# Kernel tuning notes

Measured on AMD Instinct MI355X. Metric: run time of the kernel, lower is better.

Reference implementation:

```python
import jax, jax.numpy as jnp
import numpy as np
import math

EMBED = 512
NUM_CLASSES = 100000
BATCH = 512
SCALE = 64.0
MARGIN = 0.5
COS_M = math.cos(MARGIN)
SIN_M = math.sin(MARGIN)
THRESHOLD = math.cos(math.pi - MARGIN)
MARGIN_MULT = math.sin(math.pi - MARGIN) * MARGIN
EPS = 1e-12  # F.normalize eps


def setup_inputs() -> dict:
    key = jax.random.key(0)
    k1, k2, k3 = jax.random.split(key, 3)
    embeddings = jax.random.normal(k1, (BATCH, EMBED), dtype=jnp.float32)
    labels = jax.random.randint(k2, (BATCH,), 0, NUM_CLASSES, dtype=jnp.int64)
    # xavier-uniform-like init for weight (num_classes, embedding_size)
    limit = math.sqrt(6.0 / (NUM_CLASSES + EMBED))
    weight = jax.random.uniform(k3, (NUM_CLASSES, EMBED), dtype=jnp.float32,
                                minval=-limit, maxval=limit)
    return {"embeddings": embeddings, "labels": labels, "weight": weight}


def _l2_normalize(x, axis):
    norm = jnp.sqrt(jnp.sum(x * x, axis=axis, keepdims=True))
    return x / jnp.maximum(norm, EPS)


def reference(embeddings, labels, weight):
    e = _l2_normalize(embeddings, axis=1)          # (B, D)
    w = _l2_normalize(weight, axis=1)              # (C, D)
    cosine = jnp.einsum('bd,cd->bc', e, w)         # (B, C)
    sine = jnp.sqrt(jnp.clip(1.0 - cosine * cosine, 0.0, None))
    phi = cosine * COS_M - sine * SIN_M
    # easy_margin=False branch
    phi = jnp.where(cosine > THRESHOLD, phi, cosine - MARGIN_MULT)
    one_hot = jax.nn.one_hot(labels, NUM_CLASSES, dtype=cosine.dtype)
    logits = SCALE * (one_hot * phi + (1.0 - one_hot) * cosine)
    logp = jax.nn.log_softmax(logits, axis=1)      # (B, C)
    nll = -jnp.take_along_axis(logp, labels[:, None], axis=1)[:, 0]
    return jnp.mean(nll)
```

## Files before the change

kernel.cpp:

```cpp
#include <hip/hip_runtime.h>
#include <hip/hip_bf16.h>
#include <math.h>

#define BATCH 512
#define EMBED 512
#define NCLS  100000
#define NT128 782
#define NCG   128
#define NBLK  256

typedef __attribute__((ext_vector_type(4)))  float f32x4;
typedef __attribute__((ext_vector_type(16))) float f32x16;
typedef __attribute__((ext_vector_type(2)))  long  i64x2;

constexpr float kCOS_M = 0.8775825618903728f;
constexpr float kSIN_M = 0.4794255386042030f;
constexpr float kTHR   = -0.8775825618903728f;
constexpr float kMM    = 0.2397127693021015f;

#define BARRIER() asm volatile("s_waitcnt lgkmcnt(0)\n\ts_barrier" ::: "memory")

__device__ __forceinline__ unsigned cvt4(float a, float b, float c, float d) {
  int v = __builtin_amdgcn_cvt_pk_fp8_f32(a, b, 0, false);
  v = __builtin_amdgcn_cvt_pk_fp8_f32(c, d, v, true);
  return (unsigned)v;
}

__global__ void knorm_e(const float* __restrict__ E, unsigned char* __restrict__ En8) {
  int r = blockIdx.x;
  int l = threadIdx.x;
  const f32x4* src = (const f32x4*)(E + r * EMBED);
  f32x4 a = src[2 * l], b = src[2 * l + 1];
  float ss = a.x*a.x + a.y*a.y + a.z*a.z + a.w*a.w
           + b.x*b.x + b.y*b.y + b.z*b.z + b.w*b.w;
#pragma unroll
  for (int d = 1; d < 64; d <<= 1) ss += __shfl_xor(ss, d);
  float s = 16.0f / fmaxf(sqrtf(ss), 1e-12f);
  uint2 pk;
  pk.x = cvt4(a.x * s, a.y * s, a.z * s, a.w * s);
  pk.y = cvt4(b.x * s, b.y * s, b.z * s, b.w * s);
  int slotL = (l & 1) * 16 + (l >> 2);
  int half  = (l >> 1) & 1;
  *(uint2*)(En8 + r * 512 + (((slotL ^ (r & 31)) << 4) | (half << 3))) = pk;
}

__global__ void klabel(const float* __restrict__ E, const float* __restrict__ W,
                       const int* __restrict__ labels,
                       float* __restrict__ lcos, float* __restrict__ lphi)
{
  int r = blockIdx.x * 8 + (threadIdx.x >> 6);
  int l = threadIdx.x & 63;
  int lbl = labels[r];
  const float* ep = E + (size_t)r * EMBED + l * 8;
  const float* wp = W + (size_t)lbl * EMBED + l * 8;
  f32x4 e0 = *(const f32x4*)ep, e1 = *(const f32x4*)(ep + 4);
  f32x4 w0 = *(const f32x4*)wp, w1 = *(const f32x4*)(wp + 4);
  float dot = e0.x*w0.x + e0.y*w0.y + e0.z*w0.z + e0.w*w0.w
            + e1.x*w1.x + e1.y*w1.y + e1.z*w1.z + e1.w*w1.w;
  float se = e0.x*e0.x + e0.y*e0.y + e0.z*e0.z + e0.w*e0.w
           + e1.x*e1.x + e1.y*e1.y + e1.z*e1.z + e1.w*e1.w;
  float sw = w0.x*w0.x + w0.y*w0.y + w0.z*w0.z + w0.w*w0.w
           + w1.x*w1.x + w1.y*w1.y + w1.z*w1.z + w1.w*w1.w;
#pragma unroll
  for (int d = 1; d < 64; d <<= 1) {
    dot += __shfl_xor(dot, d); se += __shfl_xor(se, d); sw += __shfl_xor(sw, d);
  }
  float cosv = dot / (fmaxf(sqrtf(se), 1e-12f) * fmaxf(sqrtf(sw), 1e-12f));
  float cc = fminf(fmaxf(cosv, -1.f), 1.f);
  float sine = sqrtf(fmaxf(1.f - cc * cc, 0.f));
  float phi = (cosv > kTHR) ? (cosv * kCOS_M - sine * kSIN_M) : (cosv - kMM);
  if (l == 0) { lcos[r] = 64.f * cosv; lphi[r] = 64.f * phi; }
}

__global__ __launch_bounds__(1024, 4) void kmain(
    const unsigned char* __restrict__ En8, const float* __restrict__ W,
    float* __restrict__ psum)
{
  __shared__ __align__(16) unsigned char Asm[256 * 512];
  __shared__ __align__(16) unsigned char Bsm[2][8192];
  __shared__ float rowsum[128];
  __shared__ float smemS[2][256];

  int bid = blockIdx.x;
  int xcd = bid & 7;
  int panel = (bid >> 3) & 1;
  int grp = bid >> 4;
  int cg = xcd | (grp << 3);

  int tid = threadIdx.x;
  int w = tid >> 6, l = tid & 63;
  int wr = w >> 1, wc = w & 1;
  int cl = l & 31, hi = l >> 5;
  int bcls = tid >> 3, bs3 = tid & 7;

  int nt = (NT128 - cg + 127) >> 7;
  int nph = nt * 8;

#pragma unroll
  for (int i = 0; i < 8; ++i) {
    int base = i * 16384 + w * 1024;
    __builtin_amdgcn_global_load_lds(
        (const __attribute__((address_space(1))) void*)(En8 + panel * 131072 + base + l * 16),
        (__attribute__((address_space(3))) void*)(&Asm[base]), 16, 0, 0);
  }

  float ssq = 0.f;
  const int boff = (bcls >> 6) * 4096
                 + ((bs3 & 1) * 2 + (bs3 >> 2)) * 1024
                 + (bcls & 63) * 16 + ((bs3 >> 1) & 1) * 8;

  f32x4 Ra0, Ra1, Rb0, Rb1;
  auto loadB = [&](int q, f32x4& v0, f32x4& v1) {
    int cls = (cg + ((q >> 3) << 7)) * 128 + bcls;
    if (cls >= NCLS) cls = NCLS - 1;
    const float* p = W + (size_t)cls * EMBED + (q & 7) * 64 + bs3 * 8;
    v0 = *(const f32x4*)p;
    v1 = *(const f32x4*)(p + 4);
  };
  auto writeB = [&](int buf, f32x4 v0, f32x4 v1) {
    float x0 = v0.x*128.f, x1 = v0.y*128.f, x2 = v0.z*128.f, x3 = v0.w*128.f;
    float x4 = v1.x*128.f, x5 = v1.y*128.f, x6 = v1.z*128.f, x7 = v1.w*128.f;
    ssq += x0*x0 + x1*x1 + x2*x2 + x3*x3 + x4*x4 + x5*x5 + x6*x6 + x7*x7;
    uint2 pk;
    pk.x = cvt4(x0, x1, x2, x3);
    pk.y = cvt4(x4, x5, x6, x7);
    *(uint2*)(&Bsm[buf][boff]) = pk;
  };

  f32x16 acc0, acc1, S;
#pragma unroll
  for (int e = 0; e < 16; ++e) { acc0[e] = 0.f; acc1[e] = 0.f; S[e] = 0.f; }

  const unsigned char* Abase = &Asm[(wr * 32 + cl) * 512];
  const unsigned char* Bc0 = &Bsm[0][wc * 4096 + (hi * 2) * 1024 + cl * 16];
  const unsigned char* Bc1 = &Bsm[1][wc * 4096 + (hi * 2) * 1024 + cl * 16];

  auto compute = [&](const unsigned char* bb, int pt) {
    int t0 = pt * 2;
    i64x2 a0 = *(const i64x2*)(Abase + ((((hi << 4) | t0)       ^ cl) << 4));
    i64x2 a1 = *(const i64x2*)(Abase + ((((hi << 4) | (t0 + 1)) ^ cl) << 4));
    i64x2 b0 = *(const i64x2*)(bb);
    i64x2 b1 = *(const i64x2*)(bb + 1024);
    i64x2 c0 = *(const i64x2*)(bb + 512);
    i64x2 c1 = *(const i64x2*)(bb + 1024 + 512);
    acc0 = __builtin_amdgcn_mfma_f32_32x32x16_fp8_fp8(a0[0], b0[0], acc0, 0, 0, 0);
    acc0 = __builtin_amdgcn_mfma_f32_32x32x16_fp8_fp8(a0[1], b0[1], acc0, 0, 0, 0);
    acc0 = __builtin_amdgcn_mfma_f32_32x32x16_fp8_fp8(a1[0], b1[0], acc0, 0, 0, 0);
    acc0 = __builtin_amdgcn_mfma_f32_32x32x16_fp8_fp8(a1[1], b1[1], acc0, 0, 0, 0);
    acc1 = __builtin_amdgcn_mfma_f32_32x32x16_fp8_fp8(a0[0], c0[0], acc1, 0, 0, 0);
    acc1 = __builtin_amdgcn_mfma_f32_32x32x16_fp8_fp8(a0[1], c0[1], acc1, 0, 0, 0);
    acc1 = __builtin_amdgcn_mfma_f32_32x32x16_fp8_fp8(a1[0], c1[0], acc1, 0, 0, 0);
    acc1 = __builtin_amdgcn_mfma_f32_32x32x16_fp8_fp8(a1[1], c1[1], acc1, 0, 0, 0);
  };

  auto ssqred = [&]() {
    float sq = ssq;
    sq += __shfl_xor(sq, 1); sq += __shfl_xor(sq, 2); sq += __shfl_xor(sq, 4);
    if (bs3 == 0) rowsum[bcls] = sq;
    ssq = 0.f;
  };

  auto epilogue = [&](int T) {
    int base = (cg + (T << 7)) * 128 + wc * 64;
    float rs0 = fmaxf(rowsum[wc * 64 + cl], 1e-30f);
    float rs1 = fmaxf(rowsum[wc * 64 + 32 + cl], 1e-30f);
    float rn0 = 4.0f / sqrtf(rs0);
    float rn1 = 4.0f / sqrtf(rs1);
    float vm0 = (base + cl < NCLS) ? 1.0f : 0.0f;
    float vm1 = (base + 32 + cl < NCLS) ? 1.0f : 0.0f;
#pragma unroll
    for (int e = 0; e < 16; ++e) {
      float u0 = __expf(fmaf(acc0[e], rn0, -64.0f));
      float u1 = __expf(fmaf(acc1[e], rn1, -64.0f));
      S[e] = fmaf(u0, vm0, fmaf(u1, vm1, S[e]));
      acc0[e] = 0.f; acc1[e] = 0.f;
    }
  };

  loadB(0, Ra0, Ra1); loadB(1, Rb0, Rb1);
  writeB(0, Ra0, Ra1); writeB(1, Rb0, Rb1);
  loadB(2, Ra0, Ra1); loadB(3, Rb0, Rb1);
  asm volatile("s_waitcnt vmcnt(0)" ::: "memory");
  BARRIER();

  for (int p = 0; p < nph; p += 2) {
    compute(Bc0, p & 7);
    BARRIER();
    if (p + 2 < nph) writeB(0, Ra0, Ra1);
    if (p + 4 < nph) loadB(p + 4, Ra0, Ra1);
    int po = p + 1;
    compute(Bc1, po & 7);
    if ((po & 7) == 7) epilogue(po >> 3);
    BARRIER();
    if (po + 2 < nph) writeB(1, Rb0, Rb1);
    if (po + 4 < nph) loadB(po + 4, Rb0, Rb1);
    if (((po + 2) & 7) == 7) ssqred();
  }

#pragma unroll
  for (int e = 0; e < 16; ++e) {
    float v = S[e];
    v += __shfl_xor(v, 1); v += __shfl_xor(v, 2); v += __shfl_xor(v, 4);
    v += __shfl_xor(v, 8); v += __shfl_xor(v, 16);
    S[e] = v;
  }
  __syncthreads();
  if (cl == 0) {
#pragma unroll
    for (int e = 0; e < 16; ++e) {
      int row = wr * 32 + (e & 3) + 8 * (e >> 2) + 4 * hi;
      smemS[wc][row] = S[e];
    }
  }
  __syncthreads();
  if (tid < 256) psum[bid * 256 + tid] = smemS[0][tid] + smemS[1][tid];
}

__global__ void kred1(const float* __restrict__ psum, float* __restrict__ pp2) {
  int g = blockIdx.x;
  int r = threadIdx.x;
  int panel = g >> 4, grp = g & 15;
  float s = 0.f;
#pragma unroll
  for (int x = 0; x < 8; ++x) {
    int bid = x | (panel << 3) | (grp << 4);
    s += psum[bid * 256 + r];
  }
  pp2[g * 256 + r] = s;
}

__global__ void kfinal(const float* __restrict__ pp2, const float* __restrict__ lcos,
                       const float* __restrict__ lphi, float* __restrict__ out)
{
  int tid = threadIdx.x;
  int panel = tid >> 8, rl = tid & 255;
  float S = 0.f;
#pragma unroll
  for (int grp = 0; grp < 16; ++grp)
    S += pp2[((panel << 4) | grp) * 256 + rl];
  float lc = lcos[tid], lp = lphi[tid];
  S = S - __expf(lc - 64.f) + __expf(lp - 64.f);
  float nll = 64.f + __logf(S) - lp;
#pragma unroll
  for (int d = 1; d < 64; d <<= 1) nll += __shfl_xor(nll, d);
  __shared__ float sm[8];
  if ((tid & 63) == 0) sm[tid >> 6] = nll;
  __syncthreads();
  if (tid == 0) {
    float t = 0.f;
    for (int k = 0; k < 8; ++k) t += sm[k];
    out[0] = t * (1.0f / 512.0f);
  }
}

extern "C" void kernel_launch(void* const* d_in, const int* in_sizes, int n_in,
                              void* d_out, int out_size, void* d_ws, size_t ws_size,
                              hipStream_t stream)
{
  const float* E      = (const float*)d_in[0];
  const int*   labels = (const int*)d_in[1];
  const float* W      = (const float*)d_in[2];
  float* out = (float*)d_out;

  char* ws = (char*)d_ws;
  unsigned char* En8 = (unsigned char*)ws;
  float* psum = (float*)(ws + 262144);
  float* pp2  = (float*)(ws + 524288);
  float* lcos = (float*)(ws + 557056);
  float* lphi = lcos + BATCH;

  knorm_e<<<BATCH, 64, 0, stream>>>(E, En8);
  klabel <<<64, 512, 0, stream>>>(E, W, labels, lcos, lphi);
  kmain  <<<NBLK, 1024, 0, stream>>>(En8, W, psum);
  kred1  <<<32, 256, 0, stream>>>(psum, pp2);
  kfinal <<<1, 512, 0, stream>>>(pp2, lcos, lphi, out);
}
```

Measured before the change: 80.83 us.

## Split batch into four 128-row panels and stream A tiles per phase

```diff
diff --git a/kernel.cpp b/kernel.cpp
--- a/kernel.cpp
+++ b/kernel.cpp
@@ -6,8 +6,7 @@
 #define EMBED 512
 #define NCLS  100000
 #define NT128 782
-#define NCG   128
-#define NBLK  256
+#define NBLK  512
 
 typedef __attribute__((ext_vector_type(4)))  float f32x4;
 typedef __attribute__((ext_vector_type(16))) float f32x16;
@@ -39,9 +38,8 @@
   uint2 pk;
   pk.x = cvt4(a.x * s, a.y * s, a.z * s, a.w * s);
   pk.y = cvt4(b.x * s, b.y * s, b.z * s, b.w * s);
-  int slotL = (l & 1) * 16 + (l >> 2);
-  int half  = (l >> 1) & 1;
-  *(uint2*)(En8 + r * 512 + (((slotL ^ (r & 31)) << 4) | (half << 3))) = pk;
+  int t = l >> 2, hi = l & 1, hf = (l >> 1) & 1;
+  *(uint2*)(En8 + ((((t << 1) | hi) * 512 + r) << 4) + hf * 8) = pk;
 }
 
 __global__ void klabel(const float* __restrict__ E, const float* __restrict__ W,
@@ -72,91 +70,99 @@
   if (l == 0) { lcos[r] = 64.f * cosv; lphi[r] = 64.f * phi; }
 }
 
-__global__ __launch_bounds__(1024, 4) void kmain(
+__global__ __launch_bounds__(512, 4) void kmain(
     const unsigned char* __restrict__ En8, const float* __restrict__ W,
     float* __restrict__ psum)
 {
-  __shared__ __align__(16) unsigned char Asm[256 * 512];
+  __shared__ __align__(16) unsigned char Asm[2][8192];
   __shared__ __align__(16) unsigned char Bsm[2][8192];
   __shared__ float rowsum[128];
-  __shared__ float smemS[2][256];
+  __shared__ float smemS[2][128];
 
   int bid = blockIdx.x;
   int xcd = bid & 7;
-  int panel = (bid >> 3) & 1;
-  int grp = bid >> 4;
+  int panel = (bid >> 3) & 3;
+  int grp = bid >> 5;
   int cg = xcd | (grp << 3);
 
   int tid = threadIdx.x;
   int w = tid >> 6, l = tid & 63;
   int wr = w >> 1, wc = w & 1;
   int cl = l & 31, hi = l >> 5;
-  int bcls = tid >> 3, bs3 = tid & 7;
-
-  int nt = (NT128 - cg + 127) >> 7;
+  int bcls = tid >> 2, bs = tid & 3;
+
+  int nt = (cg < 14) ? 7 : 6;
   int nph = nt * 8;
 
-#pragma unroll
-  for (int i = 0; i < 8; ++i) {
-    int base = i * 16384 + w * 1024;
+  int ac = tid >> 7, ar = tid & 127;
+  auto stageA = [&](int q) {
+    int t = ((q & 7) << 1) | (ac >> 1);
+    int hh = ac & 1;
+    const unsigned char* src = En8 + ((((t << 1) | hh) * 512 + panel * 128 + ar) << 4);
     __builtin_amdgcn_global_load_lds(
-        (const __attribute__((address_space(1))) void*)(En8 + panel * 131072 + base + l * 16),
-        (__attribute__((address_space(3))) void*)(&Asm[base]), 16, 0, 0);
-  }
+        (const __attribute__((address_space(1))) void*)src,
+        (__attribute__((address_space(3))) void*)(&Asm[q & 1][tid * 16]), 16, 0, 0);
+  };
 
   float ssq = 0.f;
-  const int boff = (bcls >> 6) * 4096
-                 + ((bs3 & 1) * 2 + (bs3 >> 2)) * 1024
-                 + (bcls & 63) * 16 + ((bs3 >> 1) & 1) * 8;
-
-  f32x4 Ra0, Ra1, Rb0, Rb1;
-  auto loadB = [&](int q, f32x4& v0, f32x4& v1) {
-    int cls = (cg + ((q >> 3) << 7)) * 128 + bcls;
+  const int tp = bs >> 1, hf = bs & 1;
+  const int wbase0 = (((tp << 1) | 0) * 128 + bcls) * 16 + hf * 8;
+  const int wbase1 = wbase0 + 2048;
+
+  f32x4 Ra[4], Rb[4];
+  auto loadB = [&](int q, f32x4* R) {
+    int T = q >> 3;
+    int cls = (cg + (T << 7)) * 128 + bcls;
     if (cls >= NCLS) cls = NCLS - 1;
-    const float* p = W + (size_t)cls * EMBED + (q & 7) * 64 + bs3 * 8;
-    v0 = *(const f32x4*)p;
-    v1 = *(const f32x4*)(p + 4);
-  };
-  auto writeB = [&](int buf, f32x4 v0, f32x4 v1) {
-    float x0 = v0.x*128.f, x1 = v0.y*128.f, x2 = v0.z*128.f, x3 = v0.w*128.f;
-    float x4 = v1.x*128.f, x5 = v1.y*128.f, x6 = v1.z*128.f, x7 = v1.w*128.f;
-    ssq += x0*x0 + x1*x1 + x2*x2 + x3*x3 + x4*x4 + x5*x5 + x6*x6 + x7*x7;
-    uint2 pk;
-    pk.x = cvt4(x0, x1, x2, x3);
-    pk.y = cvt4(x4, x5, x6, x7);
-    *(uint2*)(&Bsm[buf][boff]) = pk;
+    const float* p = W + (size_t)cls * EMBED + ((q & 7) << 6) + (bs << 4);
+#pragma unroll
+    for (int i = 0; i < 4; ++i) R[i] = *(const f32x4*)(p + i * 4);
+  };
+  auto writeB = [&](int buf, f32x4* R) {
+#pragma unroll
+    for (int i = 0; i < 4; ++i)
+      ssq += R[i].x*R[i].x + R[i].y*R[i].y + R[i].z*R[i].z + R[i].w*R[i].w;
+    uint2 p0, p1;
+    p0.x = cvt4(R[0].x*128.f, R[0].y*128.f, R[0].z*128.f, R[0].w*128.f);
+    p0.y = cvt4(R[1].x*128.f, R[1].y*128.f, R[1].z*128.f, R[1].w*128.f);
+    p1.x = cvt4(R[2].x*128.f, R[2].y*128.f, R[2].z*128.f, R[2].w*128.f);
+    p1.y = cvt4(R[3].x*128.f, R[3].y*128.f, R[3].z*128.f, R[3].w*128.f);
+    *(uint2*)(&Bsm[buf][wbase0]) = p0;
+    *(uint2*)(&Bsm[buf][wbase1]) = p1;
   };
 
   f32x16 acc0, acc1, S;
 #pragma unroll
   for (int e = 0; e < 16; ++e) { acc0[e] = 0.f; acc1[e] = 0.f; S[e] = 0.f; }
 
-  const unsigned char* Abase = &Asm[(wr * 32 + cl) * 512];
-  const unsigned char* Bc0 = &Bsm[0][wc * 4096 + (hi * 2) * 1024 + cl * 16];
-  const unsigned char* Bc1 = &Bsm[1][wc * 4096 + (hi * 2) * 1024 + cl * 16];
-
-  auto compute = [&](const unsigned char* bb, int pt) {
-    int t0 = pt * 2;
-    i64x2 a0 = *(const i64x2*)(Abase + ((((hi << 4) | t0)       ^ cl) << 4));
-    i64x2 a1 = *(const i64x2*)(Abase + ((((hi << 4) | (t0 + 1)) ^ cl) << 4));
-    i64x2 b0 = *(const i64x2*)(bb);
-    i64x2 b1 = *(const i64x2*)(bb + 1024);
-    i64x2 c0 = *(const i64x2*)(bb + 512);
-    i64x2 c1 = *(const i64x2*)(bb + 1024 + 512);
-    acc0 = __builtin_amdgcn_mfma_f32_32x32x16_fp8_fp8(a0[0], b0[0], acc0, 0, 0, 0);
-    acc0 = __builtin_amdgcn_mfma_f32_32x32x16_fp8_fp8(a0[1], b0[1], acc0, 0, 0, 0);
-    acc0 = __builtin_amdgcn_mfma_f32_32x32x16_fp8_fp8(a1[0], b1[0], acc0, 0, 0, 0);
-    acc0 = __builtin_amdgcn_mfma_f32_32x32x16_fp8_fp8(a1[1], b1[1], acc0, 0, 0, 0);
-    acc1 = __builtin_amdgcn_mfma_f32_32x32x16_fp8_fp8(a0[0], c0[0], acc1, 0, 0, 0);
-    acc1 = __builtin_amdgcn_mfma_f32_32x32x16_fp8_fp8(a0[1], c0[1], acc1, 0, 0, 0);
-    acc1 = __builtin_amdgcn_mfma_f32_32x32x16_fp8_fp8(a1[0], c1[0], acc1, 0, 0, 0);
-    acc1 = __builtin_amdgcn_mfma_f32_32x32x16_fp8_fp8(a1[1], c1[1], acc1, 0, 0, 0);
+  const int aoff = hi * 2048 + (wr * 32 + cl) * 16;
+  const int boff = hi * 2048 + (wc * 64 + cl) * 16;
+
+  auto compute = [&](int buf) {
+    const unsigned char* A = &Asm[buf][0];
+    const unsigned char* B = &Bsm[buf][0];
+    i64x2 a0  = *(const i64x2*)(A + aoff);
+    i64x2 a1  = *(const i64x2*)(A + aoff + 4096);
+    i64x2 b00 = *(const i64x2*)(B + boff);
+    i64x2 b01 = *(const i64x2*)(B + boff + 512);
+    i64x2 b10 = *(const i64x2*)(B + boff + 4096);
+    i64x2 b11 = *(const i64x2*)(B + boff + 4096 + 512);
+    __builtin_amdgcn_s_setprio(1);
+    acc0 = __builtin_amdgcn_mfma_f32_32x32x16_fp8_fp8(a0[0], b00[0], acc0, 0, 0, 0);
+    acc0 = __builtin_amdgcn_mfma_f32_32x32x16_fp8_fp8(a0[1], b00[1], acc0, 0, 0, 0);
+    acc1 = __builtin_amdgcn_mfma_f32_32x32x16_fp8_fp8(a0[0], b01[0], acc1, 0, 0, 0);
+    acc1 = __builtin_amdgcn_mfma_f32_32x32x16_fp8_fp8(a0[1], b01[1], acc1, 0, 0, 0);
+    acc0 = __builtin_amdgcn_mfma_f32_32x32x16_fp8_fp8(a1[0], b10[0], acc0, 0, 0, 0);
+    acc0 = __builtin_amdgcn_mfma_f32_32x32x16_fp8_fp8(a1[1], b10[1], acc0, 0, 0, 0);
+    acc1 = __builtin_amdgcn_mfma_f32_32x32x16_fp8_fp8(a1[0], b11[0], acc1, 0, 0, 0);
+    acc1 = __builtin_amdgcn_mfma_f32_32x32x16_fp8_fp8(a1[1], b11[1], acc1, 0, 0, 0);
+    __builtin_amdgcn_s_setprio(0);
   };
 
   auto ssqred = [&]() {
     float sq = ssq;
-    sq += __shfl_xor(sq, 1); sq += __shfl_xor(sq, 2); sq += __shfl_xor(sq, 4);
-    if (bs3 == 0) rowsum[bcls] = sq;
+    sq += __shfl_xor(sq, 1); sq += __shfl_xor(sq, 2);
+    if (bs == 0) rowsum[bcls] = sq;
     ssq = 0.f;
   };
 
@@ -164,8 +170,8 @@
     int base = (cg + (T << 7)) * 128 + wc * 64;
     float rs0 = fmaxf(rowsum[wc * 64 + cl], 1e-30f);
     float rs1 = fmaxf(rowsum[wc * 64 + 32 + cl], 1e-30f);
-    float rn0 = 4.0f / sqrtf(rs0);
-    float rn1 = 4.0f / sqrtf(rs1);
+    float rn0 = 0.03125f * rsqrtf(rs0);
+    float rn1 = 0.03125f * rsqrtf(rs1);
     float vm0 = (base + cl < NCLS) ? 1.0f : 0.0f;
     float vm1 = (base + 32 + cl < NCLS) ? 1.0f : 0.0f;
 #pragma unroll
@@ -177,24 +183,28 @@
     }
   };
 
-  loadB(0, Ra0, Ra1); loadB(1, Rb0, Rb1);
-  writeB(0, Ra0, Ra1); writeB(1, Rb0, Rb1);
-  loadB(2, Ra0, Ra1); loadB(3, Rb0, Rb1);
+  stageA(0);
+  loadB(0, Ra); loadB(1, Rb);
   asm volatile("s_waitcnt vmcnt(0)" ::: "memory");
+  writeB(0, Ra);
+  loadB(2, Ra);
   BARRIER();
 
   for (int p = 0; p < nph; p += 2) {
-    compute(Bc0, p & 7);
+    writeB(1, Rb);
+    stageA(p + 1);
+    loadB(p + 3, Rb);
+    if (((p + 1) & 7) == 7) ssqred();
+    asm volatile("s_waitcnt vmcnt(4)" ::: "memory");
+    compute(0);
     BARRIER();
-    if (p + 2 < nph) writeB(0, Ra0, Ra1);
-    if (p + 4 < nph) loadB(p + 4, Ra0, Ra1);
-    int po = p + 1;
-    compute(Bc1, po & 7);
-    if ((po & 7) == 7) epilogue(po >> 3);
+    writeB(0, Ra);
+    stageA(p + 2);
+    loadB(p + 4, Ra);
+    asm volatile("s_waitcnt vmcnt(4)" ::: "memory");
+    compute(1);
+    if (((p + 1) & 7) == 7) epilogue((p + 1) >> 3);
     BARRIER();
-    if (po + 2 < nph) writeB(1, Rb0, Rb1);
-    if (po + 4 < nph) loadB(po + 4, Rb0, Rb1);
-    if (((po + 2) & 7) == 7) ssqred();
   }
 
 #pragma unroll
@@ -213,7 +223,7 @@
     }
   }
   __syncthreads();
-  if (tid < 256) psum[bid * 256 + tid] = smemS[0][tid] + smemS[1][tid];
+  if (tid < 128) psum[bid * 128 + tid] = smemS[0][tid] + smemS[1][tid];
 }
 
 __global__ void kred1(const float* __restrict__ psum, float* __restrict__ pp2) {
@@ -223,21 +233,21 @@
   float s = 0.f;
 #pragma unroll
   for (int x = 0; x < 8; ++x) {
-    int bid = x | (panel << 3) | (grp << 4);
-    s += psum[bid * 256 + r];
-  }
-  pp2[g * 256 + r] = s;
+    int bid = x | (panel << 3) | (grp << 5);
+    s += psum[bid * 128 + r];
+  }
+  pp2[g * 128 + r] = s;
 }
 
 __global__ void kfinal(const float* __restrict__ pp2, const float* __restrict__ lcos,
                        const float* __restrict__ lphi, float* __restrict__ out)
 {
   int tid = threadIdx.x;
-  int panel = tid >> 8, rl = tid & 255;
+  int panel = tid >> 7, rl = tid & 127;
   float S = 0.f;
 #pragma unroll
   for (int grp = 0; grp < 16; ++grp)
-    S += pp2[((panel << 4) | grp) * 256 + rl];
+    S += pp2[(panel * 16 + grp) * 128 + rl];
   float lc = lcos[tid], lp = lphi[tid];
   S = S - __expf(lc - 64.f) + __expf(lp - 64.f);
   float nll = 64.f + __logf(S) - lp;
@@ -271,7 +281,7 @@
 
   knorm_e<<<BATCH, 64, 0, stream>>>(E, En8);
   klabel <<<64, 512, 0, stream>>>(E, W, labels, lcos, lphi);
-  kmain  <<<NBLK, 1024, 0, stream>>>(En8, W, psum);
-  kred1  <<<32, 256, 0, stream>>>(psum, pp2);
+  kmain  <<<NBLK, 512, 0, stream>>>(En8, W, psum);
+  kred1  <<<64, 128, 0, stream>>>(psum, pp2);
   kfinal <<<1, 512, 0, stream>>>(pp2, lcos, lphi, out);
 }
```

New measurement: 102.9 us. 27.4% more time.

## Split batch into four 128-row panels with smaller blocks and global rowsum

Applied to the files above, without the earlier changes.

```diff
diff --git a/kernel.cpp b/kernel.cpp
--- a/kernel.cpp
+++ b/kernel.cpp
@@ -6,8 +6,7 @@
 #define EMBED 512
 #define NCLS  100000
 #define NT128 782
-#define NCG   128
-#define NBLK  256
+#define NBLK  512
 
 typedef __attribute__((ext_vector_type(4)))  float f32x4;
 typedef __attribute__((ext_vector_type(16))) float f32x16;
@@ -72,59 +71,59 @@
   if (l == 0) { lcos[r] = 64.f * cosv; lphi[r] = 64.f * phi; }
 }
 
-__global__ __launch_bounds__(1024, 4) void kmain(
+__global__ __launch_bounds__(512, 4) void kmain(
     const unsigned char* __restrict__ En8, const float* __restrict__ W,
-    float* __restrict__ psum)
-{
-  __shared__ __align__(16) unsigned char Asm[256 * 512];
+    float* __restrict__ psum, float* __restrict__ rowsumG)
+{
+  __shared__ __align__(16) unsigned char Asm[128 * 512];
   __shared__ __align__(16) unsigned char Bsm[2][8192];
-  __shared__ float rowsum[128];
-  __shared__ float smemS[2][256];
 
   int bid = blockIdx.x;
   int xcd = bid & 7;
-  int panel = (bid >> 3) & 1;
-  int grp = bid >> 4;
+  int panel = (bid >> 3) & 3;
+  int grp = bid >> 5;
   int cg = xcd | (grp << 3);
 
   int tid = threadIdx.x;
   int w = tid >> 6, l = tid & 63;
   int wr = w >> 1, wc = w & 1;
   int cl = l & 31, hi = l >> 5;
-  int bcls = tid >> 3, bs3 = tid & 7;
-
-  int nt = (NT128 - cg + 127) >> 7;
+  int bcls = tid >> 2, bs2 = tid & 3;
+
+  int nt = (cg < 14) ? 7 : 6;
   int nph = nt * 8;
 
 #pragma unroll
   for (int i = 0; i < 8; ++i) {
-    int base = i * 16384 + w * 1024;
+    int base = i * 8192 + w * 1024;
     __builtin_amdgcn_global_load_lds(
-        (const __attribute__((address_space(1))) void*)(En8 + panel * 131072 + base + l * 16),
+        (const __attribute__((address_space(1))) void*)(En8 + panel * 65536 + base + l * 16),
         (__attribute__((address_space(3))) void*)(&Asm[base]), 16, 0, 0);
   }
 
   float ssq = 0.f;
-  const int boff = (bcls >> 6) * 4096
-                 + ((bs3 & 1) * 2 + (bs3 >> 2)) * 1024
-                 + (bcls & 63) * 16 + ((bs3 >> 1) & 1) * 8;
-
-  f32x4 Ra0, Ra1, Rb0, Rb1;
-  auto loadB = [&](int q, f32x4& v0, f32x4& v1) {
+  const int boffA = (bcls >> 6) * 4096 + (bs2 >> 1) * 1024 + (bcls & 63) * 16 + (bs2 & 1) * 8;
+
+  f32x4 Ra[4], Rb[4];
+  auto loadB = [&](int q, f32x4* R) {
     int cls = (cg + ((q >> 3) << 7)) * 128 + bcls;
     if (cls >= NCLS) cls = NCLS - 1;
-    const float* p = W + (size_t)cls * EMBED + (q & 7) * 64 + bs3 * 8;
-    v0 = *(const f32x4*)p;
-    v1 = *(const f32x4*)(p + 4);
-  };
-  auto writeB = [&](int buf, f32x4 v0, f32x4 v1) {
-    float x0 = v0.x*128.f, x1 = v0.y*128.f, x2 = v0.z*128.f, x3 = v0.w*128.f;
-    float x4 = v1.x*128.f, x5 = v1.y*128.f, x6 = v1.z*128.f, x7 = v1.w*128.f;
-    ssq += x0*x0 + x1*x1 + x2*x2 + x3*x3 + x4*x4 + x5*x5 + x6*x6 + x7*x7;
-    uint2 pk;
-    pk.x = cvt4(x0, x1, x2, x3);
-    pk.y = cvt4(x4, x5, x6, x7);
-    *(uint2*)(&Bsm[buf][boff]) = pk;
+    const float* p = W + (size_t)cls * EMBED + ((q & 7) << 6) + (bs2 << 4);
+#pragma unroll
+    for (int i = 0; i < 4; ++i) R[i] = *(const f32x4*)(p + i * 4);
+  };
+  auto writeB = [&](int buf, f32x4* R) {
+    float x0 = R[0].x*128.f, x1 = R[0].y*128.f, x2 = R[0].z*128.f, x3 = R[0].w*128.f;
+    float x4 = R[1].x*128.f, x5 = R[1].y*128.f, x6 = R[1].z*128.f, x7 = R[1].w*128.f;
+    float x8 = R[2].x*128.f, x9 = R[2].y*128.f, xa = R[2].z*128.f, xb = R[2].w*128.f;
+    float xc = R[3].x*128.f, xd = R[3].y*128.f, xe = R[3].z*128.f, xf = R[3].w*128.f;
+    ssq += x0*x0 + x1*x1 + x2*x2 + x3*x3 + x4*x4 + x5*x5 + x6*x6 + x7*x7
+         + x8*x8 + x9*x9 + xa*xa + xb*xb + xc*xc + xd*xd + xe*xe + xf*xf;
+    uint2 pA, pB;
+    pA.x = cvt4(x0, x1, x2, x3); pA.y = cvt4(x4, x5, x6, x7);
+    pB.x = cvt4(x8, x9, xa, xb); pB.y = cvt4(xc, xd, xe, xf);
+    *(uint2*)(&Bsm[buf][boffA])        = pA;
+    *(uint2*)(&Bsm[buf][boffA + 2048]) = pB;
   };
 
   f32x16 acc0, acc1, S;
@@ -142,7 +141,8 @@
     i64x2 b0 = *(const i64x2*)(bb);
     i64x2 b1 = *(const i64x2*)(bb + 1024);
     i64x2 c0 = *(const i64x2*)(bb + 512);
-    i64x2 c1 = *(const i64x2*)(bb + 1024 + 512);
+    i64x2 c1 = *(const i64x2*)(bb + 1536);
+    __builtin_amdgcn_s_setprio(1);
     acc0 = __builtin_amdgcn_mfma_f32_32x32x16_fp8_fp8(a0[0], b0[0], acc0, 0, 0, 0);
     acc0 = __builtin_amdgcn_mfma_f32_32x32x16_fp8_fp8(a0[1], b0[1], acc0, 0, 0, 0);
     acc0 = __builtin_amdgcn_mfma_f32_32x32x16_fp8_fp8(a1[0], b1[0], acc0, 0, 0, 0);
@@ -151,21 +151,22 @@
     acc1 = __builtin_amdgcn_mfma_f32_32x32x16_fp8_fp8(a0[1], c0[1], acc1, 0, 0, 0);
     acc1 = __builtin_amdgcn_mfma_f32_32x32x16_fp8_fp8(a1[0], c1[0], acc1, 0, 0, 0);
     acc1 = __builtin_amdgcn_mfma_f32_32x32x16_fp8_fp8(a1[1], c1[1], acc1, 0, 0, 0);
+    __builtin_amdgcn_s_setprio(0);
   };
 
   auto ssqred = [&]() {
     float sq = ssq;
-    sq += __shfl_xor(sq, 1); sq += __shfl_xor(sq, 2); sq += __shfl_xor(sq, 4);
-    if (bs3 == 0) rowsum[bcls] = sq;
+    sq += __shfl_xor(sq, 1); sq += __shfl_xor(sq, 2);
+    if (bs2 == 0) rowsumG[bid * 128 + bcls] = sq;
     ssq = 0.f;
-  };
-
+    asm volatile("s_waitcnt vmcnt(0)" ::: "memory");
+  };
+
+  float Rrs0 = 1.0f, Rrs1 = 1.0f;
   auto epilogue = [&](int T) {
+    float rn0 = 4.0f / sqrtf(fmaxf(Rrs0, 1e-30f));
+    float rn1 = 4.0f / sqrtf(fmaxf(Rrs1, 1e-30f));
     int base = (cg + (T << 7)) * 128 + wc * 64;
-    float rs0 = fmaxf(rowsum[wc * 64 + cl], 1e-30f);
-    float rs1 = fmaxf(rowsum[wc * 64 + 32 + cl], 1e-30f);
-    float rn0 = 4.0f / sqrtf(rs0);
-    float rn1 = 4.0f / sqrtf(rs1);
     float vm0 = (base + cl < NCLS) ? 1.0f : 0.0f;
     float vm1 = (base + 32 + cl < NCLS) ? 1.0f : 0.0f;
 #pragma unroll
@@ -177,24 +178,28 @@
     }
   };
 
-  loadB(0, Ra0, Ra1); loadB(1, Rb0, Rb1);
-  writeB(0, Ra0, Ra1); writeB(1, Rb0, Rb1);
-  loadB(2, Ra0, Ra1); loadB(3, Rb0, Rb1);
+  loadB(0, Ra); loadB(1, Rb);
+  writeB(0, Ra); writeB(1, Rb);
+  loadB(2, Ra); loadB(3, Rb);
   asm volatile("s_waitcnt vmcnt(0)" ::: "memory");
   BARRIER();
 
   for (int p = 0; p < nph; p += 2) {
     compute(Bc0, p & 7);
     BARRIER();
-    if (p + 2 < nph) writeB(0, Ra0, Ra1);
-    if (p + 4 < nph) loadB(p + 4, Ra0, Ra1);
+    if (p + 2 < nph) writeB(0, Ra);
+    if (p + 4 < nph) loadB(p + 4, Ra);
+    if ((p & 7) == 6) {
+      Rrs0 = rowsumG[bid * 128 + wc * 64 + cl];
+      Rrs1 = rowsumG[bid * 128 + wc * 64 + 32 + cl];
+    }
     int po = p + 1;
     compute(Bc1, po & 7);
     if ((po & 7) == 7) epilogue(po >> 3);
     BARRIER();
-    if (po + 2 < nph) writeB(1, Rb0, Rb1);
-    if (po + 4 < nph) loadB(po + 4, Rb0, Rb1);
+    if (po + 2 < nph) writeB(1, Rb);
     if (((po + 2) & 7) == 7) ssqred();
+    if (po + 4 < nph) loadB(po + 4, Rb);
   }
 
 #pragma unroll
@@ -204,16 +209,13 @@
     v += __shfl_xor(v, 8); v += __shfl_xor(v, 16);
     S[e] = v;
   }
-  __syncthreads();
   if (cl == 0) {
 #pragma unroll
     for (int e = 0; e < 16; ++e) {
       int row = wr * 32 + (e & 3) + 8 * (e >> 2) + 4 * hi;
-      smemS[wc][row] = S[e];
+      psum[bid * 256 + wc * 128 + row] = S[e];
     }
   }
-  __syncthreads();
-  if (tid < 256) psum[bid * 256 + tid] = smemS[0][tid] + smemS[1][tid];
 }
 
 __global__ void kred1(const float* __restrict__ psum, float* __restrict__ pp2) {
@@ -223,21 +225,21 @@
   float s = 0.f;
 #pragma unroll
   for (int x = 0; x < 8; ++x) {
-    int bid = x | (panel << 3) | (grp << 4);
-    s += psum[bid * 256 + r];
-  }
-  pp2[g * 256 + r] = s;
+    int bid = x | (panel << 3) | (grp << 5);
+    s += psum[bid * 256 + r] + psum[bid * 256 + 128 + r];
+  }
+  pp2[g * 128 + r] = s;
 }
 
 __global__ void kfinal(const float* __restrict__ pp2, const float* __restrict__ lcos,
                        const float* __restrict__ lphi, float* __restrict__ out)
 {
   int tid = threadIdx.x;
-  int panel = tid >> 8, rl = tid & 255;
+  int panel = tid >> 7, rl = tid & 127;
   float S = 0.f;
 #pragma unroll
   for (int grp = 0; grp < 16; ++grp)
-    S += pp2[((panel << 4) | grp) * 256 + rl];
+    S += pp2[(panel * 16 + grp) * 128 + rl];
   float lc = lcos[tid], lp = lphi[tid];
   S = S - __expf(lc - 64.f) + __expf(lp - 64.f);
   float nll = 64.f + __logf(S) - lp;
@@ -264,14 +266,15 @@
 
   char* ws = (char*)d_ws;
   unsigned char* En8 = (unsigned char*)ws;
-  float* psum = (float*)(ws + 262144);
-  float* pp2  = (float*)(ws + 524288);
-  float* lcos = (float*)(ws + 557056);
-  float* lphi = lcos + BATCH;
+  float* psum    = (float*)(ws + 262144);
+  float* rowsumG = (float*)(ws + 786432);
+  float* pp2     = (float*)(ws + 1048576);
+  float* lcos    = (float*)(ws + 1081344);
+  float* lphi    = lcos + BATCH;
 
   knorm_e<<<BATCH, 64, 0, stream>>>(E, En8);
   klabel <<<64, 512, 0, stream>>>(E, W, labels, lcos, lphi);
-  kmain  <<<NBLK, 1024, 0, stream>>>(En8, W, psum);
-  kred1  <<<32, 256, 0, stream>>>(psum, pp2);
+  kmain  <<<NBLK, 512, 0, stream>>>(En8, W, psum, rowsumG);
+  kred1  <<<64, 128, 0, stream>>>(psum, pp2);
   kfinal <<<1, 512, 0, stream>>>(pp2, lcos, lphi, out);
 }
```

New measurement: 90.84 us. 1.12x slower.

## Quad-buffer B tiles in LDS and halve barriers per phase pair

Applied to the files above, without the earlier changes.

```diff
diff --git a/kernel.cpp b/kernel.cpp
--- a/kernel.cpp
+++ b/kernel.cpp
@@ -6,7 +6,6 @@
 #define EMBED 512
 #define NCLS  100000
 #define NT128 782
-#define NCG   128
 #define NBLK  256
 
 typedef __attribute__((ext_vector_type(4)))  float f32x4;
@@ -74,12 +73,14 @@
 
 __global__ __launch_bounds__(1024, 4) void kmain(
     const unsigned char* __restrict__ En8, const float* __restrict__ W,
-    float* __restrict__ psum)
-{
-  __shared__ __align__(16) unsigned char Asm[256 * 512];
-  __shared__ __align__(16) unsigned char Bsm[2][8192];
-  __shared__ float rowsum[128];
-  __shared__ float smemS[2][256];
+    float* __restrict__ psum, float* __restrict__ rowsumG)
+{
+  __shared__ __align__(16) unsigned char SH[163840];
+  unsigned char* Asm = SH;
+  unsigned char* Bb0 = SH + 131072;
+  unsigned char* Bb1 = SH + 131072 + 8192;
+  unsigned char* Bb2 = SH + 131072 + 16384;
+  unsigned char* Bb3 = SH + 131072 + 24576;
 
   int bid = blockIdx.x;
   int xcd = bid & 7;
@@ -93,8 +94,9 @@
   int cl = l & 31, hi = l >> 5;
   int bcls = tid >> 3, bs3 = tid & 7;
 
-  int nt = (NT128 - cg + 127) >> 7;
+  int nt = (cg < 14) ? 7 : 6;
   int nph = nt * 8;
+  int R = nt * 4;
 
 #pragma unroll
   for (int i = 0; i < 8; ++i) {
@@ -105,35 +107,36 @@
   }
 
   float ssq = 0.f;
-  const int boff = (bcls >> 6) * 4096
-                 + ((bs3 & 1) * 2 + (bs3 >> 2)) * 1024
-                 + (bcls & 63) * 16 + ((bs3 >> 1) & 1) * 8;
-
-  f32x4 Ra0, Ra1, Rb0, Rb1;
+  const int boffA = (bcls >> 6) * 4096 + ((bs3 & 1) * 2 + (bs3 >> 2)) * 1024
+                  + (bcls & 63) * 16 + ((bs3 >> 1) & 1) * 8;
+
   auto loadB = [&](int q, f32x4& v0, f32x4& v1) {
     int cls = (cg + ((q >> 3) << 7)) * 128 + bcls;
     if (cls >= NCLS) cls = NCLS - 1;
-    const float* p = W + (size_t)cls * EMBED + (q & 7) * 64 + bs3 * 8;
+    const float* p = W + (size_t)cls * EMBED + ((q & 7) << 6) + bs3 * 8;
     v0 = *(const f32x4*)p;
     v1 = *(const f32x4*)(p + 4);
   };
-  auto writeB = [&](int buf, f32x4 v0, f32x4 v1) {
+  auto writeB = [&](unsigned char* buf, f32x4 v0, f32x4 v1) {
     float x0 = v0.x*128.f, x1 = v0.y*128.f, x2 = v0.z*128.f, x3 = v0.w*128.f;
     float x4 = v1.x*128.f, x5 = v1.y*128.f, x6 = v1.z*128.f, x7 = v1.w*128.f;
     ssq += x0*x0 + x1*x1 + x2*x2 + x3*x3 + x4*x4 + x5*x5 + x6*x6 + x7*x7;
     uint2 pk;
     pk.x = cvt4(x0, x1, x2, x3);
     pk.y = cvt4(x4, x5, x6, x7);
-    *(uint2*)(&Bsm[buf][boff]) = pk;
+    *(uint2*)(buf + boffA) = pk;
   };
 
   f32x16 acc0, acc1, S;
 #pragma unroll
   for (int e = 0; e < 16; ++e) { acc0[e] = 0.f; acc1[e] = 0.f; S[e] = 0.f; }
 
-  const unsigned char* Abase = &Asm[(wr * 32 + cl) * 512];
-  const unsigned char* Bc0 = &Bsm[0][wc * 4096 + (hi * 2) * 1024 + cl * 16];
-  const unsigned char* Bc1 = &Bsm[1][wc * 4096 + (hi * 2) * 1024 + cl * 16];
+  const unsigned char* Abase = Asm + (wr * 32 + cl) * 512;
+  const int bcol = wc * 4096 + hi * 2048 + cl * 16;
+  const unsigned char* Bc0 = Bb0 + bcol;
+  const unsigned char* Bc1 = Bb1 + bcol;
+  const unsigned char* Bc2 = Bb2 + bcol;
+  const unsigned char* Bc3 = Bb3 + bcol;
 
   auto compute = [&](const unsigned char* bb, int pt) {
     int t0 = pt * 2;
@@ -142,7 +145,8 @@
     i64x2 b0 = *(const i64x2*)(bb);
     i64x2 b1 = *(const i64x2*)(bb + 1024);
     i64x2 c0 = *(const i64x2*)(bb + 512);
-    i64x2 c1 = *(const i64x2*)(bb + 1024 + 512);
+    i64x2 c1 = *(const i64x2*)(bb + 1536);
+    __builtin_amdgcn_s_setprio(1);
     acc0 = __builtin_amdgcn_mfma_f32_32x32x16_fp8_fp8(a0[0], b0[0], acc0, 0, 0, 0);
     acc0 = __builtin_amdgcn_mfma_f32_32x32x16_fp8_fp8(a0[1], b0[1], acc0, 0, 0, 0);
     acc0 = __builtin_amdgcn_mfma_f32_32x32x16_fp8_fp8(a1[0], b1[0], acc0, 0, 0, 0);
@@ -151,21 +155,22 @@
     acc1 = __builtin_amdgcn_mfma_f32_32x32x16_fp8_fp8(a0[1], c0[1], acc1, 0, 0, 0);
     acc1 = __builtin_amdgcn_mfma_f32_32x32x16_fp8_fp8(a1[0], c1[0], acc1, 0, 0, 0);
     acc1 = __builtin_amdgcn_mfma_f32_32x32x16_fp8_fp8(a1[1], c1[1], acc1, 0, 0, 0);
+    __builtin_amdgcn_s_setprio(0);
   };
 
   auto ssqred = [&]() {
     float sq = ssq;
     sq += __shfl_xor(sq, 1); sq += __shfl_xor(sq, 2); sq += __shfl_xor(sq, 4);
-    if (bs3 == 0) rowsum[bcls] = sq;
+    if (bs3 == 0) rowsumG[bid * 128 + bcls] = sq;
     ssq = 0.f;
-  };
-
+    asm volatile("s_waitcnt vmcnt(0)" ::: "memory");
+  };
+
+  float Rrs0 = 1.0f, Rrs1 = 1.0f;
   auto epilogue = [&](int T) {
+    float rn0 = 4.0f / sqrtf(fmaxf(Rrs0, 1e-30f));
+    float rn1 = 4.0f / sqrtf(fmaxf(Rrs1, 1e-30f));
     int base = (cg + (T << 7)) * 128 + wc * 64;
-    float rs0 = fmaxf(rowsum[wc * 64 + cl], 1e-30f);
-    float rs1 = fmaxf(rowsum[wc * 64 + 32 + cl], 1e-30f);
-    float rn0 = 4.0f / sqrtf(rs0);
-    float rn1 = 4.0f / sqrtf(rs1);
     float vm0 = (base + cl < NCLS) ? 1.0f : 0.0f;
     float vm1 = (base + 32 + cl < NCLS) ? 1.0f : 0.0f;
 #pragma unroll
@@ -177,24 +182,41 @@
     }
   };
 
-  loadB(0, Ra0, Ra1); loadB(1, Rb0, Rb1);
-  writeB(0, Ra0, Ra1); writeB(1, Rb0, Rb1);
-  loadB(2, Ra0, Ra1); loadB(3, Rb0, Rb1);
+  f32x4 Ae0, Ae1, Ao0, Ao1, Be0, Be1, Bo0, Bo1;
+
+  loadB(0, Ae0, Ae1); loadB(1, Ao0, Ao1);
+  writeB(Bb0, Ae0, Ae1); writeB(Bb1, Ao0, Ao1);
+  loadB(2, Ae0, Ae1); loadB(3, Ao0, Ao1);
+  loadB(4, Be0, Be1); loadB(5, Bo0, Bo1);
   asm volatile("s_waitcnt vmcnt(0)" ::: "memory");
   BARRIER();
 
-  for (int p = 0; p < nph; p += 2) {
-    compute(Bc0, p & 7);
-    BARRIER();
-    if (p + 2 < nph) writeB(0, Ra0, Ra1);
-    if (p + 4 < nph) loadB(p + 4, Ra0, Ra1);
-    int po = p + 1;
-    compute(Bc1, po & 7);
-    if ((po & 7) == 7) epilogue(po >> 3);
-    BARRIER();
-    if (po + 2 < nph) writeB(1, Rb0, Rb1);
-    if (po + 4 < nph) loadB(po + 4, Rb0, Rb1);
-    if (((po + 2) & 7) == 7) ssqred();
+  for (int k = 0; k < R; k += 2) {
+    {
+      int p0 = 2 * k;
+      compute(Bc0, p0 & 7);
+      compute(Bc1, (p0 + 1) & 7);
+      if (k < R - 1) { writeB(Bb2, Ae0, Ae1); writeB(Bb3, Ao0, Ao1); }
+      if ((k & 3) == 2) ssqred();
+      loadB(p0 + 6, Ae0, Ae1);
+      loadB(p0 + 7, Ao0, Ao1);
+      BARRIER();
+    }
+    {
+      int p0 = 2 * k + 2;
+      bool epi = ((p0 + 1) & 7) == 7;
+      if (epi) {
+        Rrs0 = rowsumG[bid * 128 + wc * 64 + cl];
+        Rrs1 = rowsumG[bid * 128 + wc * 64 + 32 + cl];
+      }
+      compute(Bc2, p0 & 7);
+      compute(Bc3, (p0 + 1) & 7);
+      if (epi) epilogue((p0 + 1) >> 3);
+      if (k < R - 2) { writeB(Bb0, Be0, Be1); writeB(Bb1, Bo0, Bo1); }
+      loadB(p0 + 6, Be0, Be1);
+      loadB(p0 + 7, Bo0, Bo1);
+      BARRIER();
+    }
   }
 
 #pragma unroll
@@ -204,16 +226,13 @@
     v += __shfl_xor(v, 8); v += __shfl_xor(v, 16);
     S[e] = v;
   }
-  __syncthreads();
   if (cl == 0) {
 #pragma unroll
     for (int e = 0; e < 16; ++e) {
       int row = wr * 32 + (e & 3) + 8 * (e >> 2) + 4 * hi;
-      smemS[wc][row] = S[e];
-    }
-  }
-  __syncthreads();
-  if (tid < 256) psum[bid * 256 + tid] = smemS[0][tid] + smemS[1][tid];
+      psum[bid * 512 + wc * 256 + row] = S[e];
+    }
+  }
 }
 
 __global__ void kred1(const float* __restrict__ psum, float* __restrict__ pp2) {
@@ -224,7 +243,7 @@
 #pragma unroll
   for (int x = 0; x < 8; ++x) {
     int bid = x | (panel << 3) | (grp << 4);
-    s += psum[bid * 256 + r];
+    s += psum[bid * 512 + r] + psum[bid * 512 + 256 + r];
   }
   pp2[g * 256 + r] = s;
 }
@@ -237,7 +256,7 @@
   float S = 0.f;
 #pragma unroll
   for (int grp = 0; grp < 16; ++grp)
-    S += pp2[((panel << 4) | grp) * 256 + rl];
+    S += pp2[(panel * 16 + grp) * 256 + rl];
   float lc = lcos[tid], lp = lphi[tid];
   S = S - __expf(lc - 64.f) + __expf(lp - 64.f);
   float nll = 64.f + __logf(S) - lp;
@@ -264,14 +283,15 @@
 
   char* ws = (char*)d_ws;
   unsigned char* En8 = (unsigned char*)ws;
-  float* psum = (float*)(ws + 262144);
-  float* pp2  = (float*)(ws + 524288);
-  float* lcos = (float*)(ws + 557056);
-  float* lphi = lcos + BATCH;
+  float* psum    = (float*)(ws + 262144);
+  float* rowsumG = (float*)(ws + 786432);
+  float* pp2     = (float*)(ws + 917504);
+  float* lcos    = (float*)(ws + 950272);
+  float* lphi    = lcos + BATCH;
 
   knorm_e<<<BATCH, 64, 0, stream>>>(E, En8);
   klabel <<<64, 512, 0, stream>>>(E, W, labels, lcos, lphi);
-  kmain  <<<NBLK, 1024, 0, stream>>>(En8, W, psum);
+  kmain  <<<NBLK, 1024, 0, stream>>>(En8, W, psum, rowsumG);
   kred1  <<<32, 256, 0, stream>>>(psum, pp2);
   kfinal <<<1, 512, 0, stream>>>(pp2, lcos, lphi, out);
 }
```

New measurement: 82.02 us. Within noise of the previous version (+1.5%).
